# Kernel tuning notes

Measured on AMD Instinct MI355X. Metric: run time of the kernel, lower is better.

## Reference

```python
import jax, jax.numpy as jnp
import numpy as np

B, N, C, H = 32, 577, 768, 12
D = C // H  # head_dim = 64


def _rotate_half(t):
    half = t.shape[-1] // 2
    return jnp.concatenate([-t[..., half:], t[..., :half]], axis=-1)


def _rope(t, sin, cos):
    # t: [B, H, N-1, D]; sin/cos: [N-1, D] broadcast over batch and heads
    return t * cos + _rotate_half(t) * sin


def setup_inputs() -> dict:
    key = jax.random.key(0)
    ks = jax.random.split(key, 5)
    x = jax.random.normal(ks[0], (B, N, C), dtype=jnp.float32)
    w_qkv = jax.random.normal(ks[1], (C, 3 * C), dtype=jnp.float32) * (1.0 / np.sqrt(C))
    b_qkv = jnp.zeros((3 * C,), dtype=jnp.float32)
    w_proj = jax.random.normal(ks[2], (C, C), dtype=jnp.float32) * (1.0 / np.sqrt(C))
    b_proj = jnp.zeros((C,), dtype=jnp.float32)
    # rotary tables for the N-1 non-CLS tokens
    pos = jnp.arange(N - 1, dtype=jnp.float32)[:, None]            # [N-1, 1]
    inv_freq = 1.0 / (10000.0 ** (jnp.arange(0, D, 2, dtype=jnp.float32) / D))  # [D/2]
    ang = pos * inv_freq[None, :]                                   # [N-1, D/2]
    ang = jnp.concatenate([ang, ang], axis=-1)                      # [N-1, D]
    rope_sin = jnp.sin(ang)
    rope_cos = jnp.cos(ang)
    return {"x": x, "w_qkv": w_qkv, "b_qkv": b_qkv, "w_proj": w_proj,
            "b_proj": b_proj, "rope_sin": rope_sin, "rope_cos": rope_cos}


def reference(x, w_qkv, b_qkv, w_proj, b_proj, rope_sin, rope_cos):
    Bx, Nx, Cx = x.shape
    qkv = x @ w_qkv + b_qkv                                   # [B, N, 3C]
    qkv = qkv.reshape(Bx, Nx, 3, H, D).transpose(2, 0, 3, 1, 4)  # [3, B, H, N, D]
    q, k, v = qkv[0], qkv[1], qkv[2]
    # RoPE only on non-CLS tokens (index 0 is CLS)
    q = jnp.concatenate([q[:, :, :1, :], _rope(q[:, :, 1:, :], rope_sin, rope_cos)], axis=2)
    k = jnp.concatenate([k[:, :, :1, :], _rope(k[:, :, 1:, :], rope_sin, rope_cos)], axis=2)
    q = q / jnp.sqrt(jnp.float32(D))
    attn = jnp.einsum("bhqd,bhkd->bhqk", q, k)               # [B, H, N, N]
    attn = jax.nn.softmax(attn.astype(jnp.float32), axis=-1).astype(x.dtype)
    out = jnp.einsum("bhqk,bhkd->bhqd", attn, v)             # [B, H, N, D]
    out = out.transpose(0, 2, 1, 3).reshape(Bx, Nx, Cx)       # [B, N, C]
    return out @ w_proj + b_proj
```

## Files before the change

### kernel.cpp

```cpp
#include <hip/hip_runtime.h>

#define Bdim 32
#define Ndim 577
#define Cdim 768
#define Hdim 12
#define Ddim 64
#define Mdim (Bdim*Ndim)
#define VSTRIDE 640
#define TSTRIDE 152
#define QSCALE 0.18033688f
#define MGRP 19

typedef __attribute__((ext_vector_type(4))) float f32x4;
typedef __attribute__((ext_vector_type(8))) __bf16 bf16x8;
typedef __attribute__((ext_vector_type(4))) __bf16 bf16x4;

__device__ __forceinline__ void gl_lds16(const __bf16* g, __bf16* l) {
  __builtin_amdgcn_global_load_lds((const __attribute__((address_space(1))) void*)g,
                                   (__attribute__((address_space(3))) void*)l, 16, 0, 0);
}

__global__ __launch_bounds__(256) void f32_to_bf16(const float4* __restrict__ in,
                                                   bf16x4* __restrict__ out, int n4) {
  int i = blockIdx.x * 256 + threadIdx.x;
  if (i < n4) {
    float4 v = in[i];
    bf16x4 o = {(__bf16)v.x, (__bf16)v.y, (__bf16)v.z, (__bf16)v.w};
    out[i] = o;
  }
}

__global__ __launch_bounds__(256) void transpose_f32_bf16(const float* __restrict__ in,
                                                          __bf16* __restrict__ out,
                                                          int R, int Cc) {
  __shared__ float tile[64][65];
  int bx = blockIdx.x * 64;
  int by = blockIdx.y * 64;
  int tx = threadIdx.x & 63, ty = threadIdx.x >> 6;
  for (int i = ty; i < 64; i += 4) {
    int r = by + i, c = bx + tx;
    tile[i][tx] = (r < R && c < Cc) ? in[(size_t)r * Cc + c] : 0.f;
  }
  __syncthreads();
  for (int i = ty; i < 64; i += 4) {
    int r = bx + i, c = by + tx;
    if (r < Cc && c < R) out[(size_t)r * R + c] = (__bf16)tile[tx][i];
  }
}

__device__ __forceinline__ void gemm_bt_core(const __bf16* __restrict__ A,
                                             const __bf16* __restrict__ BT,
                                             int m0, int n0,
                                             __bf16* As, __bf16* Bs,
                                             f32x4 acc[4][4]) {
  const int t = threadIdx.x;
  const int lane = t & 63, w = t >> 6;
  const int quad = lane >> 4, l16 = lane & 15;
  const int wm = w >> 1, wn = w & 1;

  for (int k0 = 0; k0 < 768; k0 += 64) {
    __syncthreads();
    #pragma unroll
    for (int e = 0; e < 4; ++e) {
      int h = e >> 1;
      int j = ((e & 1) << 2) | w;
      int row = j * 16 + (lane >> 2);
      int col = k0 + h * 32 + (lane & 3) * 8;
      int ar = m0 + row; if (ar > Mdim - 1) ar = Mdim - 1;
      __bf16* dstA = As + h * 4096 + j * 512 + lane * 8;
      __bf16* dstB = Bs + h * 4096 + j * 512 + lane * 8;
      gl_lds16(A  + (size_t)ar * 768 + col, dstA);
      gl_lds16(BT + (size_t)(n0 + row) * 768 + col, dstB);
    }
    __syncthreads();
    #pragma unroll
    for (int s = 0; s < 2; ++s) {
      bf16x8 a[4], b[4];
      #pragma unroll
      for (int i = 0; i < 4; ++i) {
        a[i] = *(const bf16x8*)(As + s * 4096 + (wm * 64 + i * 16 + l16) * 32 + quad * 8);
        b[i] = *(const bf16x8*)(Bs + s * 4096 + (wn * 64 + i * 16 + l16) * 32 + quad * 8);
      }
      #pragma unroll
      for (int mt = 0; mt < 4; ++mt)
        #pragma unroll
        for (int nt = 0; nt < 4; ++nt)
          acc[mt][nt] = __builtin_amdgcn_mfma_f32_16x16x32_bf16(a[mt], b[nt], acc[mt][nt], 0, 0, 0);
    }
  }
}

__device__ __forceinline__ bool xcd_decode(int lin, int nb, int mb, int& n, int& m) {
  int x8 = lin & 7;
  int rest = lin >> 3;
  n = rest % nb;
  int mg = rest / nb;
  m = mg * 8 + x8;
  return m < mb;
}

__global__ __launch_bounds__(256) void qk_kernel(const __bf16* __restrict__ x,
                                                 const __bf16* __restrict__ wqkvT,
                                                 const float* __restrict__ b_qkv,
                                                 const float* __restrict__ rs,
                                                 const float* __restrict__ rc,
                                                 __bf16* __restrict__ q,
                                                 __bf16* __restrict__ k) {
  __shared__ __bf16 As[2 * 128 * 32];
  __shared__ __bf16 Bs[2 * 128 * 32];
  int nb, mbk;
  if (!xcd_decode(blockIdx.x, 12, 145, nb, mbk)) return;
  const int n0 = nb * 128, m0 = mbk * 128;

  f32x4 acc[4][4];
  const f32x4 fz = {0.f, 0.f, 0.f, 0.f};
  for (int i = 0; i < 4; ++i) for (int j = 0; j < 4; ++j) acc[i][j] = fz;
  gemm_bt_core(x, wqkvT, m0, n0, As, Bs, acc);

  const int lane = threadIdx.x & 63, w = threadIdx.x >> 6;
  const int quad = lane >> 4, l16 = lane & 15;
  const int wm = w >> 1, wn = w & 1;
  const int colbase = n0 + wn * 64;
  const int matrix = colbase / 768;
  const int head = (colbase % 768) / 64;

  #pragma unroll
  for (int mt = 0; mt < 4; ++mt) {
    int mbase = m0 + wm * 64 + mt * 16 + quad * 4;
    #pragma unroll
    for (int r = 0; r < 4; ++r) {
      int m = mbase + r;
      if (m >= Mdim) continue;
      int bb = m / 577, tok = m % 577;
      #pragma unroll
      for (int nt = 0; nt < 4; ++nt) {
        int d = nt * 16 + l16;
        float val = acc[mt][nt][r] + b_qkv[colbase + d];
        if (tok > 0) {
          float partner = acc[mt][nt ^ 2][r] + b_qkv[colbase + (d ^ 32)];
          float sn = rs[(size_t)(tok - 1) * 64 + d];
          float cs = rc[(size_t)(tok - 1) * 64 + d];
          float rot = (d < 32) ? -partner : partner;
          val = val * cs + rot * sn;
        }
        __bf16* dst;
        if (matrix == 0) { val *= QSCALE; dst = q; } else dst = k;
        dst[((size_t)(bb * 12 + head) * 577 + tok) * 64 + d] = (__bf16)val;
      }
    }
  }
}

__global__ __launch_bounds__(256) void v_kernel(const __bf16* __restrict__ x,
                                                const __bf16* __restrict__ wqkvT,
                                                const float* __restrict__ b_qkv,
                                                __bf16* __restrict__ vt) {
  __shared__ __bf16 As[2 * 128 * 32];
  __shared__ __bf16 Bs[2 * 128 * 32];
  __shared__ __bf16 Ts[64 * TSTRIDE];
  int nb, mbk;
  if (!xcd_decode(blockIdx.x, 6, 145, nb, mbk)) return;
  const int n0 = 1536 + nb * 128, m0 = mbk * 128;

  f32x4 acc[4][4];
  const f32x4 fz = {0.f, 0.f, 0.f, 0.f};
  for (int i = 0; i < 4; ++i) for (int j = 0; j < 4; ++j) acc[i][j] = fz;
  gemm_bt_core(x, wqkvT, m0, n0, As, Bs, acc);

  const int t = threadIdx.x;
  const int lane = t & 63, w = t >> 6;
  const int quad = lane >> 4, l16 = lane & 15;
  const int wm = w >> 1, wn = w & 1;
  const int colbase = n0 + wn * 64;

  #pragma unroll
  for (int h = 0; h < 2; ++h) {
    __syncthreads();
    if (wn == h) {
      #pragma unroll
      for (int mt = 0; mt < 4; ++mt) {
        int tokbase = wm * 64 + mt * 16 + quad * 4;
        #pragma unroll
        for (int r = 0; r < 4; ++r) {
          #pragma unroll
          for (int nt = 0; nt < 4; ++nt) {
            int dl = nt * 16 + l16;
            Ts[dl * TSTRIDE + tokbase + r] =
                (__bf16)(acc[mt][nt][r] + b_qkv[colbase + dl]);
          }
        }
      }
    }
    __syncthreads();
    int hh = (n0 + h * 64 - 1536) / 64;
    #pragma unroll
    for (int it = 0; it < 4; ++it) {
      int c = it * 256 + t;
      int dl = c >> 4, chunk = c & 15;
      bf16x8 vv = *(const bf16x8*)(Ts + dl * TSTRIDE + chunk * 8);
      #pragma unroll
      for (int j = 0; j < 8; ++j) {
        int m = m0 + chunk * 8 + j;
        if (m < Mdim) {
          int bb = m / 577, tok = m % 577;
          vt[((size_t)(bb * 12 + hh) * 64 + dl) * VSTRIDE + tok] = vv[j];
        }
      }
    }
  }
}

__global__ __launch_bounds__(256) void attn_kernel(const __bf16* __restrict__ q,
                                                   const __bf16* __restrict__ k,
                                                   const __bf16* __restrict__ vt,
                                                   __bf16* __restrict__ ao) {
  __shared__ __bf16 qs[4096];
  __shared__ __bf16 ks[4096];
  __shared__ __bf16 vs[4096];
  __shared__ __bf16 ps[64 * 72];

  const int x8 = blockIdx.x & 7;
  const int rest = blockIdx.x >> 3;
  const int qt = rest % 10;
  const int bh = (rest / 10) * 8 + x8;

  const int t = threadIdx.x;
  const int lane = t & 63, w = t >> 6;
  const int quad = lane >> 4, l16 = lane & 15;

  const __bf16* qbase = q + (size_t)bh * 577 * 64;
  const __bf16* kbase = k + (size_t)bh * 577 * 64;
  const __bf16* vbase = vt + (size_t)bh * 64 * VSTRIDE;

  #pragma unroll
  for (int p = 0; p < 2; ++p) {
    int g = p * 256 + t;
    int d8 = g >> 6, tok = g & 63;
    gl_lds16(qbase + (size_t)(qt * 64 + tok) * 64 + d8 * 8, qs + (size_t)g * 8);
  }

  bf16x8 kreg[2], vreg[2];
  #pragma unroll
  for (int p = 0; p < 2; ++p) {
    int g = p * 256 + t;
    kreg[p] = *(const bf16x8*)(kbase + (size_t)(g & 63) * 64 + (g >> 6) * 8);
    vreg[p] = *(const bf16x8*)(vbase + (size_t)(g & 63) * VSTRIDE + (g >> 6) * 8);
  }

  f32x4 O[4]; const f32x4 fz = {0.f, 0.f, 0.f, 0.f};
  for (int i = 0; i < 4; ++i) O[i] = fz;
  float l_part[4] = {0.f, 0.f, 0.f, 0.f};

  for (int kt = 0; kt < 10; ++kt) {
    __syncthreads();
    #pragma unroll
    for (int p = 0; p < 2; ++p) {
      int g = p * 256 + t;
      *(bf16x8*)(ks + (size_t)g * 8) = kreg[p];
      *(bf16x8*)(vs + (size_t)g * 8) = vreg[p];
    }
    __syncthreads();

    if (kt < 9) {
      #pragma unroll
      for (int p = 0; p < 2; ++p) {
        int g = p * 256 + t;
        kreg[p] = *(const bf16x8*)(kbase + (size_t)((kt + 1) * 64 + (g & 63)) * 64 + (g >> 6) * 8);
        vreg[p] = *(const bf16x8*)(vbase + (size_t)(g & 63) * VSTRIDE + (kt + 1) * 64 + (g >> 6) * 8);
      }
      __builtin_amdgcn_sched_barrier(0);
    }

    f32x4 S[4]; for (int i = 0; i < 4; ++i) S[i] = fz;
    __builtin_amdgcn_s_setprio(1);
    #pragma unroll
    for (int step = 0; step < 2; ++step) {
      bf16x8 a = *(const bf16x8*)(qs + (size_t)((step * 4 + quad) * 64 + w * 16 + l16) * 8);
      #pragma unroll
      for (int nt = 0; nt < 4; ++nt) {
        bf16x8 b = *(const bf16x8*)(ks + (size_t)((step * 4 + quad) * 64 + nt * 16 + l16) * 8);
        S[nt] = __builtin_amdgcn_mfma_f32_16x16x32_bf16(a, b, S[nt], 0, 0, 0);
      }
    }
    __builtin_amdgcn_s_setprio(0);

    int kv_left = 577 - kt * 64;
    if (kv_left < 64) {
      #pragma unroll
      for (int nt = 0; nt < 4; ++nt) {
        int c = nt * 16 + l16;
        if (c >= kv_left) { S[nt][0] = -1e30f; S[nt][1] = -1e30f; S[nt][2] = -1e30f; S[nt][3] = -1e30f; }
      }
    }

    #pragma unroll
    for (int r = 0; r < 4; ++r) {
      #pragma unroll
      for (int nt = 0; nt < 4; ++nt) {
        float e = exp2f(S[nt][r]);
        l_part[r] += e;
        ps[(size_t)(w * 16 + quad * 4 + r) * 72 + nt * 16 + l16] = (__bf16)e;
      }
    }

    __builtin_amdgcn_s_setprio(1);
    #pragma unroll
    for (int step = 0; step < 2; ++step) {
      bf16x8 a = *(const bf16x8*)(ps + (size_t)(w * 16 + l16) * 72 + step * 32 + quad * 8);
      #pragma unroll
      for (int dt = 0; dt < 4; ++dt) {
        bf16x8 b = *(const bf16x8*)(vs + (size_t)((step * 4 + quad) * 64 + dt * 16 + l16) * 8);
        O[dt] = __builtin_amdgcn_mfma_f32_16x16x32_bf16(a, b, O[dt], 0, 0, 0);
      }
    }
    __builtin_amdgcn_s_setprio(0);
  }

  const int bb = bh / 12, hh = bh % 12;
  const int qrow0 = qt * 64 + w * 16 + quad * 4;
  #pragma unroll
  for (int r = 0; r < 4; ++r) {
    float l = l_part[r];
    l += __shfl_xor(l, 1); l += __shfl_xor(l, 2);
    l += __shfl_xor(l, 4); l += __shfl_xor(l, 8);
    int row = qrow0 + r;
    if (row < 577) {
      float inv = 1.f / l;
      size_t base = ((size_t)(bb * 577 + row)) * 768 + hh * 64;
      #pragma unroll
      for (int dt = 0; dt < 4; ++dt)
        ao[base + dt * 16 + l16] = (__bf16)(O[dt][r] * inv);
    }
  }
}

__global__ __launch_bounds__(256) void proj_kernel(const __bf16* __restrict__ ao,
                                                   const __bf16* __restrict__ wprojT,
                                                   const float* __restrict__ b_proj,
                                                   float* __restrict__ out) {
  __shared__ __bf16 As[2 * 128 * 32];
  __shared__ __bf16 Bs[2 * 128 * 32];
  int nb, mbk;
  if (!xcd_decode(blockIdx.x, 6, 145, nb, mbk)) return;
  const int n0 = nb * 128, m0 = mbk * 128;

  f32x4 acc[4][4];
  const f32x4 fz = {0.f, 0.f, 0.f, 0.f};
  for (int i = 0; i < 4; ++i) for (int j = 0; j < 4; ++j) acc[i][j] = fz;
  gemm_bt_core(ao, wprojT, m0, n0, As, Bs, acc);

  const int lane = threadIdx.x & 63, w = threadIdx.x >> 6;
  const int quad = lane >> 4, l16 = lane & 15;
  const int wm = w >> 1, wn = w & 1;
  const int colbase = n0 + wn * 64;

  #pragma unroll
  for (int mt = 0; mt < 4; ++mt) {
    int mbase = m0 + wm * 64 + mt * 16 + quad * 4;
    #pragma unroll
    for (int r = 0; r < 4; ++r) {
      int m = mbase + r;
      if (m >= Mdim) continue;
      #pragma unroll
      for (int nt = 0; nt < 4; ++nt) {
        int c = colbase + nt * 16 + l16;
        out[(size_t)m * 768 + c] = acc[mt][nt][r] + b_proj[c];
      }
    }
  }
}

extern "C" void kernel_launch(void* const* d_in, const int* in_sizes, int n_in,
                              void* d_out, int out_size, void* d_ws, size_t ws_size,
                              hipStream_t stream) {
  const float* x      = (const float*)d_in[0];
  const float* w_qkv  = (const float*)d_in[1];
  const float* b_qkv  = (const float*)d_in[2];
  const float* w_proj = (const float*)d_in[3];
  const float* b_proj = (const float*)d_in[4];
  const float* rsn    = (const float*)d_in[5];
  const float* rcs    = (const float*)d_in[6];
  float* out = (float*)d_out;

  constexpr size_t QK_E = (size_t)Bdim * Hdim * Ndim * Ddim;
  constexpr size_t VT_E = (size_t)Bdim * Hdim * Ddim * VSTRIDE;
  constexpr size_t AO_E = (size_t)Mdim * Cdim;
  __bf16* q      = (__bf16*)d_ws;
  __bf16* k      = q + QK_E;
  __bf16* vt     = k + QK_E;
  __bf16* ao     = vt + VT_E;
  __bf16* xb     = ao;
  __bf16* wqkvT  = ao + AO_E;
  __bf16* wprojT = wqkvT + (size_t)2304 * 768;

  f32_to_bf16<<<13848, 256, 0, stream>>>((const float4*)x, (bf16x4*)xb,
                                         (int)(AO_E / 4));
  transpose_f32_bf16<<<dim3(36, 12), 256, 0, stream>>>(w_qkv, wqkvT, 768, 2304);
  transpose_f32_bf16<<<dim3(12, 12), 256, 0, stream>>>(w_proj, wprojT, 768, 768);
  qk_kernel<<<8 * MGRP * 12, 256, 0, stream>>>(xb, wqkvT, b_qkv, rsn, rcs, q, k);
  v_kernel<<<8 * MGRP * 6, 256, 0, stream>>>(xb, wqkvT, b_qkv, vt);
  attn_kernel<<<3840, 256, 0, stream>>>(q, k, vt, ao);
  proj_kernel<<<8 * MGRP * 6, 256, 0, stream>>>(ao, wprojT, b_proj, out);
}
```

Before: 436.2 us.

## Pre-pack QKV weights into MFMA fragment layout and load B directly to registers

Adds a transpose kernel that writes the QKV weight into a fragment-major bf16 layout matching the MFMA B operand. The QKV GEMMs then read B fragments straight from global memory into registers instead of staging them through LDS, which halves LDS usage and traffic per K step. The cost is uncached, higher-latency global loads for B that each wave issues itself without cross-wave sharing, relying on L2 for reuse.

```diff
diff --git a/kernel.cpp b/kernel.cpp
--- a/kernel.cpp
+++ b/kernel.cpp
@@ -48,6 +48,72 @@
   }
 }
 
+__global__ __launch_bounds__(256) void transpose_f32_wfrag(const float* __restrict__ in,
+                                                           __bf16* __restrict__ out) {
+  __shared__ float tile[64][65];
+  int bx = blockIdx.x * 64;
+  int by = blockIdx.y * 64;
+  int tx = threadIdx.x & 63, ty = threadIdx.x >> 6;
+  #pragma unroll
+  for (int i = ty; i < 64; i += 4)
+    tile[i][tx] = in[(size_t)(by + i) * 2304 + bx + tx];
+  __syncthreads();
+  #pragma unroll
+  for (int it = 0; it < 2; ++it) {
+    int idx = it * 256 + threadIdx.x;
+    int nl = idx & 63, kc = idx >> 6;
+    bf16x8 o;
+    #pragma unroll
+    for (int j = 0; j < 8; ++j) o[j] = (__bf16)tile[kc * 8 + j][nl];
+    int n = bx + nl, kk = by + kc * 8;
+    *(bf16x8*)(out + ((size_t)(n >> 4) * 96 + (kk >> 3)) * 128 + (n & 15) * 8) = o;
+  }
+}
+
+__device__ __forceinline__ void gemm_split_core(const __bf16* __restrict__ A,
+                                                const __bf16* __restrict__ WF,
+                                                int m0, int n0,
+                                                __bf16* As, f32x4 acc[4][4]) {
+  const int t = threadIdx.x;
+  const int lane = t & 63, w = t >> 6;
+  const int quad = lane >> 4, l16 = lane & 15;
+  const int wm = w >> 1, wn = w & 1;
+  const int nb16 = (n0 >> 4) + wn * 4;
+
+  for (int k0 = 0; k0 < 768; k0 += 64) {
+    __syncthreads();
+    bf16x8 b[2][4];
+    #pragma unroll
+    for (int s = 0; s < 2; ++s)
+      #pragma unroll
+      for (int i = 0; i < 4; ++i)
+        b[s][i] = *(const bf16x8*)(WF +
+            ((size_t)(nb16 + i) * 96 + (k0 >> 3) + s * 4 + quad) * 128 + l16 * 8);
+    #pragma unroll
+    for (int e = 0; e < 4; ++e) {
+      int h = e >> 1;
+      int j = ((e & 1) << 2) | w;
+      int row = j * 16 + (lane >> 2);
+      int col = k0 + h * 32 + (lane & 3) * 8;
+      int ar = m0 + row; if (ar > Mdim - 1) ar = Mdim - 1;
+      gl_lds16(A + (size_t)ar * 768 + col, As + h * 4096 + j * 512 + lane * 8);
+    }
+    __syncthreads();
+    #pragma unroll
+    for (int s = 0; s < 2; ++s) {
+      bf16x8 a[4];
+      #pragma unroll
+      for (int i = 0; i < 4; ++i)
+        a[i] = *(const bf16x8*)(As + s * 4096 + (wm * 64 + i * 16 + l16) * 32 + quad * 8);
+      #pragma unroll
+      for (int mt = 0; mt < 4; ++mt)
+        #pragma unroll
+        for (int nt = 0; nt < 4; ++nt)
+          acc[mt][nt] = __builtin_amdgcn_mfma_f32_16x16x32_bf16(a[mt], b[s][nt], acc[mt][nt], 0, 0, 0);
+    }
+  }
+}
+
 __device__ __forceinline__ void gemm_bt_core(const __bf16* __restrict__ A,
                                              const __bf16* __restrict__ BT,
                                              int m0, int n0,
@@ -100,14 +166,13 @@
 }
 
 __global__ __launch_bounds__(256) void qk_kernel(const __bf16* __restrict__ x,
-                                                 const __bf16* __restrict__ wqkvT,
+                                                 const __bf16* __restrict__ wf,
                                                  const float* __restrict__ b_qkv,
                                                  const float* __restrict__ rs,
                                                  const float* __restrict__ rc,
                                                  __bf16* __restrict__ q,
                                                  __bf16* __restrict__ k) {
   __shared__ __bf16 As[2 * 128 * 32];
-  __shared__ __bf16 Bs[2 * 128 * 32];
   int nb, mbk;
   if (!xcd_decode(blockIdx.x, 12, 145, nb, mbk)) return;
   const int n0 = nb * 128, m0 = mbk * 128;
@@ -115,7 +180,7 @@
   f32x4 acc[4][4];
   const f32x4 fz = {0.f, 0.f, 0.f, 0.f};
   for (int i = 0; i < 4; ++i) for (int j = 0; j < 4; ++j) acc[i][j] = fz;
-  gemm_bt_core(x, wqkvT, m0, n0, As, Bs, acc);
+  gemm_split_core(x, wf, m0, n0, As, acc);
 
   const int lane = threadIdx.x & 63, w = threadIdx.x >> 6;
   const int quad = lane >> 4, l16 = lane & 15;
@@ -152,11 +217,10 @@
 }
 
 __global__ __launch_bounds__(256) void v_kernel(const __bf16* __restrict__ x,
-                                                const __bf16* __restrict__ wqkvT,
+                                                const __bf16* __restrict__ wf,
                                                 const float* __restrict__ b_qkv,
                                                 __bf16* __restrict__ vt) {
   __shared__ __bf16 As[2 * 128 * 32];
-  __shared__ __bf16 Bs[2 * 128 * 32];
   __shared__ __bf16 Ts[64 * TSTRIDE];
   int nb, mbk;
   if (!xcd_decode(blockIdx.x, 6, 145, nb, mbk)) return;
@@ -165,7 +229,7 @@
   f32x4 acc[4][4];
   const f32x4 fz = {0.f, 0.f, 0.f, 0.f};
   for (int i = 0; i < 4; ++i) for (int j = 0; j < 4; ++j) acc[i][j] = fz;
-  gemm_bt_core(x, wqkvT, m0, n0, As, Bs, acc);
+  gemm_split_core(x, wf, m0, n0, As, acc);
 
   const int t = threadIdx.x;
   const int lane = t & 63, w = t >> 6;
@@ -390,15 +454,15 @@
   __bf16* vt     = k + QK_E;
   __bf16* ao     = vt + VT_E;
   __bf16* xb     = ao;
-  __bf16* wqkvT  = ao + AO_E;
-  __bf16* wprojT = wqkvT + (size_t)2304 * 768;
+  __bf16* wqkvF  = ao + AO_E;
+  __bf16* wprojT = wqkvF + (size_t)2304 * 768;
 
   f32_to_bf16<<<13848, 256, 0, stream>>>((const float4*)x, (bf16x4*)xb,
                                          (int)(AO_E / 4));
-  transpose_f32_bf16<<<dim3(36, 12), 256, 0, stream>>>(w_qkv, wqkvT, 768, 2304);
+  transpose_f32_wfrag<<<dim3(36, 12), 256, 0, stream>>>(w_qkv, wqkvF);
   transpose_f32_bf16<<<dim3(12, 12), 256, 0, stream>>>(w_proj, wprojT, 768, 768);
-  qk_kernel<<<8 * MGRP * 12, 256, 0, stream>>>(xb, wqkvT, b_qkv, rsn, rcs, q, k);
-  v_kernel<<<8 * MGRP * 6, 256, 0, stream>>>(xb, wqkvT, b_qkv, vt);
+  qk_kernel<<<8 * MGRP * 12, 256, 0, stream>>>(xb, wqkvF, b_qkv, rsn, rcs, q, k);
+  v_kernel<<<8 * MGRP * 6, 256, 0, stream>>>(xb, wqkvF, b_qkv, vt);
   attn_kernel<<<3840, 256, 0, stream>>>(q, k, vt, ao);
   proj_kernel<<<8 * MGRP * 6, 256, 0, stream>>>(ao, wprojT, b_proj, out);
 }
```

Result: no change. 432.3 us (-0.9%).
